# Performance work log

Hardware: AMD Instinct MI355X
Metric: run time of the kernel (lower is better)

Reference implementation:

```python
import jax, jax.numpy as jnp
import numpy as np

NUM_NODES = 128
BATCH = 32768
G_BASE = np.array([8.0, 8.0, 16.0, 8.0, 8.0, 4.0, 8.0, 8.0, 4.0, 4.0, 4.0, 8.0], dtype=np.float32)
T_BASE = np.array([0.02, 0.02, 0.16, 0.28], dtype=np.float32)


def setup_inputs() -> dict:
    key = jax.random.key(0)
    k1, k2, k3, k4, k5, k6 = jax.random.split(key, 6)
    x = jax.random.normal(k1, (BATCH, NUM_NODES * 8), dtype=jnp.float32)
    t = jnp.zeros((), dtype=jnp.float32)
    node_connectivity = jax.random.normal(k2, (NUM_NODES, NUM_NODES), dtype=jnp.float32) * 0.1
    # per-node gain/time-constant params (init values + small perturbation so grads are generic)
    G = jnp.asarray(G_BASE)[None, :] * (1.0 + 0.05 * jax.random.normal(k3, (NUM_NODES, 12), dtype=jnp.float32))
    T = jnp.asarray(T_BASE)[None, :] * (1.0 + 0.05 * jax.random.normal(k4, (NUM_NODES, 4), dtype=jnp.float32))
    adaptation = jnp.ones((NUM_NODES,), dtype=jnp.float32) + 0.1 * jax.random.normal(k5, (NUM_NODES,), dtype=jnp.float32)
    R = jnp.ones((NUM_NODES,), dtype=jnp.float32) + 0.1 * jax.random.normal(k6, (NUM_NODES,), dtype=jnp.float32)
    return {"t": t, "x": x, "node_connectivity": node_connectivity, "G": G, "T": T,
            "adaptation": adaptation, "R": R}


def reference(t, x, node_connectivity, G, T, adaptation, R):
    # x: [B, N*8] state; activation = sigmoid branch of FlexibleCMC
    B = x.shape[0]
    N = node_connectivity.shape[0]
    x = jnp.clip(x, -100.0, 100.0)
    xs = x.reshape(B, N, 8)  # [B, N, 8]
    # S = sigmoid(R*x) - sigmoid(0)  (sigmoid activation branch)
    S = jax.nn.sigmoid(R[None, :, None] * xs) - 0.5  # [B, N, 8]
    # message passing: mean activity of each node, weighted by connectivity (no self-loop)
    m = xs.mean(axis=-1)  # [B, N]
    C = node_connectivity * (1.0 - jnp.eye(N, dtype=node_connectivity.dtype))
    node_input = jnp.einsum('bj,ij->bi', m, C)  # [B, N]
    scale = jax.nn.sigmoid(adaptation) * 0.1  # [N]

    g = lambda k: G[:, k]  # [N], broadcasts against [B, N]
    u1 = -g(0) * S[..., 0] - g(2) * S[..., 4] - g(1) * S[..., 2] + node_input
    f1 = scale * (u1 - 2.0 * xs[..., 1] - xs[..., 0] / T[:, 0]) / T[:, 0]
    u3 = g(7) * S[..., 0] - g(6) * S[..., 2] - g(11) * S[..., 4] + node_input
    f3 = scale * (u3 - 2.0 * xs[..., 3] - xs[..., 2] / T[:, 1]) / T[:, 1]
    u5 = g(4) * S[..., 0] + g(5) * S[..., 6] - g(3) * S[..., 4] + g(10) * S[..., 2] + node_input
    f5 = scale * (u5 - 2.0 * xs[..., 5] - xs[..., 4] / T[:, 2]) / T[:, 2]
    u7 = -g(9) * S[..., 6] - g(8) * S[..., 4] + node_input
    f7 = scale * (u7 - 2.0 * xs[..., 7] - xs[..., 6] / T[:, 3]) / T[:, 3]
    f0 = scale * xs[..., 1]
    f2 = scale * xs[..., 3]
    f4 = scale * xs[..., 5]
    f6 = scale * xs[..., 7]
    f = jnp.stack([f0, f1, f2, f3, f4, f5, f6, f7], axis=-1)  # [B, N, 8]
    return f.reshape(B, N * 8)
```

## Files before the change

### kernel.cpp

```cpp
#include <hip/hip_runtime.h>

#define NNODES 128
#define BATCH  32768
#define BLOCK  256
#define ROWS_PER_CHUNK 8
#define NCHUNKS (BATCH / ROWS_PER_CHUNK)
#define GRID   1024

__device__ __forceinline__ float sigmoidf_(float z) {
    return 1.0f / (1.0f + __expf(-z));
}

__device__ __forceinline__ float clipf_(float v) {
    return fminf(fmaxf(v, -100.0f), 100.0f);
}

__device__ __forceinline__ unsigned short bf16_(float f) {
    unsigned u = __float_as_uint(f);
    return (unsigned short)((u + 0x8000u) >> 16);
}

__device__ __forceinline__ void node_update(const float* xs8, float ni,
                                            const float* gi, const float* invTi,
                                            float sci, float Ri, float* f8) {
    float S0 = sigmoidf_(Ri * xs8[0]) - 0.5f;
    float S2 = sigmoidf_(Ri * xs8[2]) - 0.5f;
    float S4 = sigmoidf_(Ri * xs8[4]) - 0.5f;
    float S6 = sigmoidf_(Ri * xs8[6]) - 0.5f;
    float u1 = ni - gi[0] * S0 - gi[1] * S2 - gi[2]  * S4;
    float u3 = ni + gi[7] * S0 - gi[6] * S2 - gi[11] * S4;
    float u5 = ni + gi[4] * S0 + gi[10] * S2 - gi[3] * S4 + gi[5] * S6;
    float u7 = ni - gi[8] * S4 - gi[9] * S6;
    f8[0] = sci * xs8[1];
    f8[1] = sci * (u1 - 2.0f * xs8[1] - xs8[0] * invTi[0]) * invTi[0];
    f8[2] = sci * xs8[3];
    f8[3] = sci * (u3 - 2.0f * xs8[3] - xs8[2] * invTi[1]) * invTi[1];
    f8[4] = sci * xs8[5];
    f8[5] = sci * (u5 - 2.0f * xs8[5] - xs8[4] * invTi[2]) * invTi[2];
    f8[6] = sci * xs8[7];
    f8[7] = sci * (u7 - 2.0f * xs8[7] - xs8[6] * invTi[3]) * invTi[3];
}

__global__ __launch_bounds__(BLOCK, 2)
void cmc_kernel(const float* __restrict__ x,
                const float* __restrict__ C,
                const float* __restrict__ G,
                const float* __restrict__ T,
                const float* __restrict__ adap,
                const float* __restrict__ R,
                float* __restrict__ out)
{
    __shared__ unsigned short ct16[NNODES * NNODES];
    __shared__ float m_lds[4][2][NNODES];

    const int tid  = threadIdx.x;
    const int lane = tid & 63;
    const int w    = tid >> 6;
    const int nA   = 2 * lane;

    {
        const int j0 = (tid & 31) * 4;
        const int tb = tid >> 5;
        #pragma unroll
        for (int it = 0; it < 4; ++it) {
            const int i0 = (tb + it * 8) * 4;
            float4 row[4];
            #pragma unroll
            for (int r = 0; r < 4; ++r)
                row[r] = *reinterpret_cast<const float4*>(C + (size_t)(i0 + r) * NNODES + j0);
            #pragma unroll
            for (int k = 0; k < 4; ++k) {
                const int j = j0 + k;
                ushort4 wv;
                wv.x = (i0 + 0 == j) ? (unsigned short)0 : bf16_((&row[0].x)[k]);
                wv.y = (i0 + 1 == j) ? (unsigned short)0 : bf16_((&row[1].x)[k]);
                wv.z = (i0 + 2 == j) ? (unsigned short)0 : bf16_((&row[2].x)[k]);
                wv.w = (i0 + 3 == j) ? (unsigned short)0 : bf16_((&row[3].x)[k]);
                const int col = i0 ^ ((j & 15) << 2);
                *reinterpret_cast<ushort4*>(&ct16[j * NNODES + col]) = wv;
            }
        }
    }

    float g[2][12], invT[2][4], sc[2], Rr[2];
    #pragma unroll
    for (int i = 0; i < 2; ++i) {
        int n = nA + i;
        #pragma unroll
        for (int k = 0; k < 12; ++k) g[i][k] = G[n * 12 + k];
        #pragma unroll
        for (int k = 0; k < 4; ++k) invT[i][k] = 1.0f / T[n * 4 + k];
        sc[i] = 0.1f * sigmoidf_(adap[n]);
        Rr[i] = R[n];
    }

    __syncthreads();

    for (int chunk = blockIdx.x; chunk < NCHUNKS; chunk += GRID) {
        const int r0 = chunk * ROWS_PER_CHUNK + 2 * w;

        float xv[2][16];
        {
            const float4* p0 = reinterpret_cast<const float4*>(x + (size_t)r0 * 1024 + lane * 16);
            const float4* p1 = reinterpret_cast<const float4*>(x + (size_t)(r0 + 1) * 1024 + lane * 16);
            #pragma unroll
            for (int q = 0; q < 4; ++q) {
                float4 v = p0[q];
                xv[0][q * 4 + 0] = clipf_(v.x); xv[0][q * 4 + 1] = clipf_(v.y);
                xv[0][q * 4 + 2] = clipf_(v.z); xv[0][q * 4 + 3] = clipf_(v.w);
            }
            #pragma unroll
            for (int q = 0; q < 4; ++q) {
                float4 v = p1[q];
                xv[1][q * 4 + 0] = clipf_(v.x); xv[1][q * 4 + 1] = clipf_(v.y);
                xv[1][q * 4 + 2] = clipf_(v.z); xv[1][q * 4 + 3] = clipf_(v.w);
            }
        }

        #pragma unroll
        for (int rr = 0; rr < 2; ++rr) {
            float s0 = 0.0f, s1 = 0.0f;
            #pragma unroll
            for (int k = 0; k < 8; ++k) { s0 += xv[rr][k]; s1 += xv[rr][8 + k]; }
            float2 mv = make_float2(s0 * 0.125f, s1 * 0.125f);
            *reinterpret_cast<float2*>(&m_lds[w][rr][nA]) = mv;
        }

        float acc00 = 0.f, acc01 = 0.f, acc10 = 0.f, acc11 = 0.f;
        #pragma unroll 4
        for (int j4 = 0; j4 < 32; ++j4) {
            float4 mA = *reinterpret_cast<const float4*>(&m_lds[w][0][j4 * 4]);
            float4 mB = *reinterpret_cast<const float4*>(&m_lds[w][1][j4 * 4]);
            const float* pmA = &mA.x; const float* pmB = &mB.x;
            #pragma unroll
            for (int c = 0; c < 4; ++c) {
                const int j   = j4 * 4 + c;
                const int col = nA ^ ((j & 15) << 2);
                unsigned cu = *reinterpret_cast<const unsigned*>(&ct16[j * NNODES + col]);
                float ce = __uint_as_float(cu << 16);
                float co = __uint_as_float(cu & 0xffff0000u);
                acc00 = fmaf(pmA[c], ce, acc00);
                acc01 = fmaf(pmA[c], co, acc01);
                acc10 = fmaf(pmB[c], ce, acc10);
                acc11 = fmaf(pmB[c], co, acc11);
            }
        }

        {
            float* o0 = out + (size_t)r0 * 1024 + lane * 16;
            float* o1 = out + (size_t)(r0 + 1) * 1024 + lane * 16;
            float f8[8];
            node_update(&xv[0][0], acc00, g[0], invT[0], sc[0], Rr[0], f8);
            *reinterpret_cast<float4*>(o0)      = make_float4(f8[0], f8[1], f8[2], f8[3]);
            *reinterpret_cast<float4*>(o0 + 4)  = make_float4(f8[4], f8[5], f8[6], f8[7]);
            node_update(&xv[0][8], acc01, g[1], invT[1], sc[1], Rr[1], f8);
            *reinterpret_cast<float4*>(o0 + 8)  = make_float4(f8[0], f8[1], f8[2], f8[3]);
            *reinterpret_cast<float4*>(o0 + 12) = make_float4(f8[4], f8[5], f8[6], f8[7]);
            node_update(&xv[1][0], acc10, g[0], invT[0], sc[0], Rr[0], f8);
            *reinterpret_cast<float4*>(o1)      = make_float4(f8[0], f8[1], f8[2], f8[3]);
            *reinterpret_cast<float4*>(o1 + 4)  = make_float4(f8[4], f8[5], f8[6], f8[7]);
            node_update(&xv[1][8], acc11, g[1], invT[1], sc[1], Rr[1], f8);
            *reinterpret_cast<float4*>(o1 + 8)  = make_float4(f8[0], f8[1], f8[2], f8[3]);
            *reinterpret_cast<float4*>(o1 + 12) = make_float4(f8[4], f8[5], f8[6], f8[7]);
        }
    }
}

extern "C" void kernel_launch(void* const* d_in, const int* in_sizes, int n_in,
                              void* d_out, int out_size, void* d_ws, size_t ws_size,
                              hipStream_t stream) {
    const float* x    = (const float*)d_in[1];
    const float* C    = (const float*)d_in[2];
    const float* G    = (const float*)d_in[3];
    const float* T    = (const float*)d_in[4];
    const float* adap = (const float*)d_in[5];
    const float* R    = (const float*)d_in[6];
    float* out        = (float*)d_out;

    hipLaunchKernelGGL(cmc_kernel, dim3(GRID), dim3(BLOCK), 0, stream,
                       x, C, G, T, adap, R, out);
}
```

Before: 64.58 us.

## Switch node-input matvec to packed fp16 dot2 with a relaid connectivity table

Stores the masked connectivity matrix in LDS as packed fp16 pairs, laid out so each lane reads one uint4 per pair of j-steps. Row means are also packed as fp16 pairs. The inner loop then uses v_dot2_f32_f16 instead of unpacking bf16 values and issuing scalar FMAs, which cuts LDS reads and VALU instructions. The cost is fp16 precision on the means (the x values are normal, so the range fits) and a different rounding mode (round toward zero).

```diff
diff --git a/kernel.cpp b/kernel.cpp
--- a/kernel.cpp
+++ b/kernel.cpp
@@ -7,17 +7,23 @@
 #define NCHUNKS (BATCH / ROWS_PER_CHUNK)
 #define GRID   1024
 
+typedef __fp16 half2_t __attribute__((ext_vector_type(2)));
+
+__device__ __forceinline__ half2_t h2_(unsigned u) {
+    union { unsigned u; half2_t h; } cv; cv.u = u; return cv.h;
+}
+__device__ __forceinline__ unsigned pk_(float a, float b) {
+    union { half2_t h; unsigned u; } cv;
+    cv.h = __builtin_amdgcn_cvt_pkrtz(a, b);
+    return cv.u;
+}
+
 __device__ __forceinline__ float sigmoidf_(float z) {
     return 1.0f / (1.0f + __expf(-z));
 }
 
 __device__ __forceinline__ float clipf_(float v) {
     return fminf(fmaxf(v, -100.0f), 100.0f);
-}
-
-__device__ __forceinline__ unsigned short bf16_(float f) {
-    unsigned u = __float_as_uint(f);
-    return (unsigned short)((u + 0x8000u) >> 16);
 }
 
 __device__ __forceinline__ void node_update(const float* xs8, float ni,
@@ -50,8 +56,8 @@
                 const float* __restrict__ R,
                 float* __restrict__ out)
 {
-    __shared__ unsigned short ct16[NNODES * NNODES];
-    __shared__ float m_lds[4][2][NNODES];
+    __shared__ uint4 ct4[32 * 64];
+    __shared__ __align__(16) uint2 m2a[4][64];
 
     const int tid  = threadIdx.x;
     const int lane = tid & 63;
@@ -59,26 +65,31 @@
     const int nA   = 2 * lane;
 
     {
-        const int j0 = (tid & 31) * 4;
-        const int tb = tid >> 5;
+        const int p   = tid & 63;
+        const int seg = tid >> 6;
+        const int c0  = seg * 32;
+        const int r0i = 2 * p, r1i = 2 * p + 1;
+        float4 qv0[8], qv1[8];
         #pragma unroll
-        for (int it = 0; it < 4; ++it) {
-            const int i0 = (tb + it * 8) * 4;
-            float4 row[4];
-            #pragma unroll
-            for (int r = 0; r < 4; ++r)
-                row[r] = *reinterpret_cast<const float4*>(C + (size_t)(i0 + r) * NNODES + j0);
-            #pragma unroll
-            for (int k = 0; k < 4; ++k) {
-                const int j = j0 + k;
-                ushort4 wv;
-                wv.x = (i0 + 0 == j) ? (unsigned short)0 : bf16_((&row[0].x)[k]);
-                wv.y = (i0 + 1 == j) ? (unsigned short)0 : bf16_((&row[1].x)[k]);
-                wv.z = (i0 + 2 == j) ? (unsigned short)0 : bf16_((&row[2].x)[k]);
-                wv.w = (i0 + 3 == j) ? (unsigned short)0 : bf16_((&row[3].x)[k]);
-                const int col = i0 ^ ((j & 15) << 2);
-                *reinterpret_cast<ushort4*>(&ct16[j * NNODES + col]) = wv;
-            }
+        for (int q = 0; q < 8; ++q) {
+            qv0[q] = *reinterpret_cast<const float4*>(C + (size_t)r0i * NNODES + c0 + 4 * q);
+            qv1[q] = *reinterpret_cast<const float4*>(C + (size_t)r1i * NNODES + c0 + 4 * q);
+        }
+        #pragma unroll
+        for (int q = 0; q < 8; ++q) {
+            const int colb = c0 + 4 * q;
+            float a0 = (r0i == colb + 0) ? 0.f : qv0[q].x;
+            float b0 = (r0i == colb + 1) ? 0.f : qv0[q].y;
+            float c0v= (r0i == colb + 2) ? 0.f : qv0[q].z;
+            float d0 = (r0i == colb + 3) ? 0.f : qv0[q].w;
+            float a1 = (r1i == colb + 0) ? 0.f : qv1[q].x;
+            float b1 = (r1i == colb + 1) ? 0.f : qv1[q].y;
+            float c1v= (r1i == colb + 2) ? 0.f : qv1[q].z;
+            float d1 = (r1i == colb + 3) ? 0.f : qv1[q].w;
+            uint4 rec;
+            rec.x = pk_(a0, b0); rec.y = pk_(c0v, d0);
+            rec.z = pk_(a1, b1); rec.w = pk_(c1v, d1);
+            ct4[(seg * 8 + q) * 64 + p] = rec;
         }
     }
 
@@ -95,6 +106,8 @@
     }
 
     __syncthreads();
+
+    uint2* m2 = &m2a[w][0];
 
     for (int chunk = blockIdx.x; chunk < NCHUNKS; chunk += GRID) {
         const int r0 = chunk * ROWS_PER_CHUNK + 2 * w;
@@ -117,38 +130,37 @@
             }
         }
 
-        #pragma unroll
-        for (int rr = 0; rr < 2; ++rr) {
-            float s0 = 0.0f, s1 = 0.0f;
+        {
+            float s00 = 0.f, s01 = 0.f, s10 = 0.f, s11 = 0.f;
             #pragma unroll
-            for (int k = 0; k < 8; ++k) { s0 += xv[rr][k]; s1 += xv[rr][8 + k]; }
-            float2 mv = make_float2(s0 * 0.125f, s1 * 0.125f);
-            *reinterpret_cast<float2*>(&m_lds[w][rr][nA]) = mv;
+            for (int k = 0; k < 8; ++k) {
+                s00 += xv[0][k]; s01 += xv[0][8 + k];
+                s10 += xv[1][k]; s11 += xv[1][8 + k];
+            }
+            uint2 mv;
+            mv.x = pk_(s00 * 0.125f, s01 * 0.125f);
+            mv.y = pk_(s10 * 0.125f, s11 * 0.125f);
+            m2[lane] = mv;
         }
 
         float acc00 = 0.f, acc01 = 0.f, acc10 = 0.f, acc11 = 0.f;
         #pragma unroll 4
-        for (int j4 = 0; j4 < 32; ++j4) {
-            float4 mA = *reinterpret_cast<const float4*>(&m_lds[w][0][j4 * 4]);
-            float4 mB = *reinterpret_cast<const float4*>(&m_lds[w][1][j4 * 4]);
-            const float* pmA = &mA.x; const float* pmB = &mB.x;
-            #pragma unroll
-            for (int c = 0; c < 4; ++c) {
-                const int j   = j4 * 4 + c;
-                const int col = nA ^ ((j & 15) << 2);
-                unsigned cu = *reinterpret_cast<const unsigned*>(&ct16[j * NNODES + col]);
-                float ce = __uint_as_float(cu << 16);
-                float co = __uint_as_float(cu & 0xffff0000u);
-                acc00 = fmaf(pmA[c], ce, acc00);
-                acc01 = fmaf(pmA[c], co, acc01);
-                acc10 = fmaf(pmB[c], ce, acc10);
-                acc11 = fmaf(pmB[c], co, acc11);
-            }
+        for (int jp2 = 0; jp2 < 32; ++jp2) {
+            uint4 mm = *reinterpret_cast<const uint4*>(&m2[2 * jp2]);
+            uint4 ct = ct4[jp2 * 64 + lane];
+            acc00 = __builtin_amdgcn_fdot2(h2_(mm.x), h2_(ct.x), acc00, false);
+            acc00 = __builtin_amdgcn_fdot2(h2_(mm.z), h2_(ct.y), acc00, false);
+            acc01 = __builtin_amdgcn_fdot2(h2_(mm.x), h2_(ct.z), acc01, false);
+            acc01 = __builtin_amdgcn_fdot2(h2_(mm.z), h2_(ct.w), acc01, false);
+            acc10 = __builtin_amdgcn_fdot2(h2_(mm.y), h2_(ct.x), acc10, false);
+            acc10 = __builtin_amdgcn_fdot2(h2_(mm.w), h2_(ct.y), acc10, false);
+            acc11 = __builtin_amdgcn_fdot2(h2_(mm.y), h2_(ct.z), acc11, false);
+            acc11 = __builtin_amdgcn_fdot2(h2_(mm.w), h2_(ct.w), acc11, false);
         }
 
         {
             float* o0 = out + (size_t)r0 * 1024 + lane * 16;
-            float* o1 = out + (size_t)(r0 + 1) * 1024 + lane * 16;
+            float* o1 = o0 + 1024;
             float f8[8];
             node_update(&xv[0][0], acc00, g[0], invT[0], sc[0], Rr[0], f8);
             *reinterpret_cast<float4*>(o0)      = make_float4(f8[0], f8[1], f8[2], f8[3]);
```

New measurement: 65.99 us. 1.02x slower.
